# Kernel tuning notes

Measured on AMD Instinct MI355X. Metric: run time of the kernel, lower is better.

Reference implementation:

```python
import jax, jax.numpy as jnp
import numpy as np

B, H, C, Q = 32, 128, 2048, 256
NEG = -1e30


def setup_inputs() -> dict:
    key = jax.random.key(0)
    ks = jax.random.split(key, 8)
    context = jax.random.normal(ks[0], (B, H, C), dtype=jnp.float32)
    question = jax.random.normal(ks[1], (B, H, Q), dtype=jnp.float32)
    context_word_mask = jax.random.randint(ks[2], (B, C), 0, 2).astype(jnp.int32)
    question_word_mask = jax.random.randint(ks[3], (B, Q), 0, 2).astype(jnp.int32)
    # trilinear similarity params (QANet): S = c.w_c + q.w_q + (c*q).w_cq + bias
    scale = 1.0 / np.sqrt(H)
    w_c = jax.random.normal(ks[4], (H,), dtype=jnp.float32) * scale
    w_q = jax.random.normal(ks[5], (H,), dtype=jnp.float32) * scale
    w_cq = jax.random.normal(ks[6], (H,), dtype=jnp.float32) * scale
    bias = jnp.zeros((), dtype=jnp.float32)
    return {"context": context, "question": question,
            "context_word_mask": context_word_mask,
            "question_word_mask": question_word_mask,
            "w_c": w_c, "w_q": w_q, "w_cq": w_cq, "bias": bias}


def reference(context, question, context_word_mask, question_word_mask, w_c, w_q, w_cq, bias):
    # context: [B,H,C], question: [B,H,Q]
    # Trilinear similarity S[b,i,j] without materializing tiled [B,C,Q,H] tensors:
    part_c = jnp.einsum('bhi,h->bi', context, w_c)            # [B,C]
    part_q = jnp.einsum('bhj,h->bj', question, w_q)           # [B,Q]
    part_cq = jnp.einsum('bhi,bhj->bij', context * w_cq[None, :, None], question)  # [B,C,Q]
    S = part_cq + part_c[:, :, None] + part_q[:, None, :] + bias  # [B,C,Q]

    q_mask = question_word_mask[:, None, :].astype(bool)      # [B,1,Q]
    c_mask = context_word_mask[:, :, None].astype(bool)       # [B,C,1]
    S_row_norm = jax.nn.softmax(jnp.where(q_mask, S, NEG), axis=2)      # softmax over Q
    S_col_norm_T = jnp.swapaxes(jax.nn.softmax(jnp.where(c_mask, S, NEG), axis=1), 1, 2)  # [B,Q,C]

    context_t = jnp.swapaxes(context, 1, 2)    # [B,C,H]
    question_t = jnp.swapaxes(question, 1, 2)  # [B,Q,H]

    c2q = jnp.swapaxes(jnp.einsum('bij,bjh->bih', S_row_norm, question_t), 1, 2)  # [B,H,C]
    q2c = jnp.swapaxes(
        jnp.einsum('bik,bkh->bih', jnp.einsum('bij,bjk->bik', S_row_norm, S_col_norm_T), context_t),
        1, 2)  # [B,H,C]
    return (context, c2q, context * c2q, context * q2c)
```

## Files before the change

### kernel.cpp

```cpp
#include <hip/hip_runtime.h>
#include <hip/hip_bf16.h>
#include <math.h>


constexpr int kB = 32, kH = 128, kC = 2048, kQ = 256;
constexpr int kColChunks = 128;
constexpr float kNEG = -1e30f;

typedef short bf16x8 __attribute__((ext_vector_type(8)));
typedef float f32x4 __attribute__((ext_vector_type(4)));

static __device__ __forceinline__ unsigned short f2bf(float f) {
    __hip_bfloat16 h = __float2bfloat16(f);
    return __builtin_bit_cast(unsigned short, h);
}
static __device__ __forceinline__ float bf2f(unsigned short u) {
    unsigned int x = ((unsigned int)u) << 16;
    return __builtin_bit_cast(float, x);
}

__global__ __launch_bounds__(256) void k_prep_c(const float* __restrict__ ctx,
                                                const float* __restrict__ w_c,
                                                const float* __restrict__ w_cq,
                                                unsigned short* __restrict__ ctxW,
                                                float* __restrict__ part_c) {
    int i0 = blockIdx.x * 64, b = blockIdx.y;
    __shared__ unsigned short tile[64 * 136];
    __shared__ float pcp[4][64];
    int t = threadIdx.x;
    int il = t & 63, hg = t >> 6, hb = hg * 2;
    float accc = 0.f;
#pragma unroll
    for (int r = 0; r < 16; ++r) {
        int h = r * 8 + hb;
        float v0 = ctx[((size_t)b * kH + h) * kC + i0 + il];
        float v1 = ctx[((size_t)b * kH + h + 1) * kC + i0 + il];
        accc += v0 * w_c[h] + v1 * w_c[h + 1];
        unsigned int pk = (unsigned int)f2bf(v0 * w_cq[h]) |
                          ((unsigned int)f2bf(v1 * w_cq[h + 1]) << 16);
        *(unsigned int*)&tile[il * 136 + h] = pk;
    }
    pcp[hg][il] = accc;
    __syncthreads();
    if (t < 64) part_c[b * kC + i0 + t] = pcp[0][t] + pcp[1][t] + pcp[2][t] + pcp[3][t];
#pragma unroll
    for (int r = 0; r < 4; ++r) {
        int idx = r * 256 + t;
        int i = idx >> 4, hc = (idx & 15) * 8;
        *(bf16x8*)&ctxW[((size_t)b * kC + i0 + i) * kH + hc] =
            *(const bf16x8*)&tile[i * 136 + hc];
    }
}

__global__ __launch_bounds__(256) void k_prep_q(const float* __restrict__ q,
                                                const float* __restrict__ w_q,
                                                unsigned short* __restrict__ qT,
                                                unsigned short* __restrict__ qB,
                                                float* __restrict__ part_q) {
    int j0 = blockIdx.x * 64, b = blockIdx.y;
    __shared__ unsigned short tile[64 * 136];
    __shared__ float pcp[4][64];
    int t = threadIdx.x;
    int jl = t & 63, hg = t >> 6, hb = hg * 2;
    float accq = 0.f;
#pragma unroll
    for (int r = 0; r < 16; ++r) {
        int h = r * 8 + hb;
        float v0 = q[((size_t)b * kH + h) * kQ + j0 + jl];
        float v1 = q[((size_t)b * kH + h + 1) * kQ + j0 + jl];
        accq += v0 * w_q[h] + v1 * w_q[h + 1];
        qB[((size_t)b * kH + h) * kQ + j0 + jl]     = f2bf(v0);
        qB[((size_t)b * kH + h + 1) * kQ + j0 + jl] = f2bf(v1);
        unsigned int pk = (unsigned int)f2bf(v0) | ((unsigned int)f2bf(v1) << 16);
        *(unsigned int*)&tile[jl * 136 + h] = pk;
    }
    pcp[hg][jl] = accq;
    __syncthreads();
    if (t < 64) part_q[b * kQ + j0 + t] = pcp[0][t] + pcp[1][t] + pcp[2][t] + pcp[3][t];
#pragma unroll
    for (int r = 0; r < 4; ++r) {
        int idx = r * 256 + t;
        int j = idx >> 4, hc = (idx & 15) * 8;
        *(bf16x8*)&qT[((size_t)b * kQ + j0 + j) * kH + hc] =
            *(const bf16x8*)&tile[j * 136 + hc];
    }
}

__global__ __launch_bounds__(256) void k_Ssoft(const unsigned short* __restrict__ ctxW,
                                               const unsigned short* __restrict__ qT,
                                               const float* __restrict__ part_c,
                                               const float* __restrict__ part_q,
                                               const float* __restrict__ bias,
                                               const int* __restrict__ qmask,
                                               const int* __restrict__ cmask,
                                               unsigned short* __restrict__ RNb,
                                               float* __restrict__ rowscale,
                                               float* __restrict__ ps) {
    int i0 = blockIdx.x * 64, b = blockIdx.y;
    __shared__ unsigned short As[64 * 40];
    __shared__ unsigned short Bs[256 * 40];
    __shared__ float smpq[256];
    __shared__ int smqm[256];
    int t = threadIdx.x;
    int lane = t & 63, w = t >> 6;
    int lrow = lane & 15, q4 = lane >> 4, kgrp = q4 * 8;
    smpq[t] = part_q[b * kQ + t];
    smqm[t] = qmask[b * kQ + t];

    f32x4 acc[16];
#pragma unroll
    for (int nt = 0; nt < 16; ++nt) acc[nt] = (f32x4){0.f, 0.f, 0.f, 0.f};

    for (int kk = 0; kk < 4; ++kk) {
        int h0 = kk * 32;
        {
            int iA = t >> 2, hcA = (t & 3) * 8;
            *(bf16x8*)&As[iA * 40 + hcA] =
                *(const bf16x8*)&ctxW[((size_t)b * kC + i0 + iA) * kH + h0 + hcA];
        }
#pragma unroll
        for (int r2 = 0; r2 < 4; ++r2) {
            int idx = r2 * 256 + t;
            int jB = idx >> 2, hcB = (idx & 3) * 8;
            *(bf16x8*)&Bs[jB * 40 + hcB] =
                *(const bf16x8*)&qT[((size_t)b * kQ + jB) * kH + h0 + hcB];
        }
        __syncthreads();
        bf16x8 af = *(const bf16x8*)&As[(w * 16 + lrow) * 40 + kgrp];
#pragma unroll
        for (int nt = 0; nt < 16; ++nt) {
            bf16x8 bf = *(const bf16x8*)&Bs[(nt * 16 + lrow) * 40 + kgrp];
            acc[nt] = __builtin_amdgcn_mfma_f32_16x16x32_bf16(af, bf, acc[nt], 0, 0, 0);
        }
        __syncthreads();
    }

    float bs = bias[0];
    float pq[16];
    int qm[16];
#pragma unroll
    for (int nt = 0; nt < 16; ++nt) {
        int col = nt * 16 + lrow;
        pq[nt] = smpq[col];
        qm[nt] = smqm[col];
    }
    int rowbase = i0 + w * 16 + q4 * 4;
    float pc[4];
    int cmr[4];
#pragma unroll
    for (int r = 0; r < 4; ++r) {
        pc[r] = part_c[b * kC + rowbase + r] + bs;
        cmr[r] = cmask[b * kC + rowbase + r];
    }
#pragma unroll
    for (int nt = 0; nt < 16; ++nt)
#pragma unroll
        for (int r = 0; r < 4; ++r)
            acc[nt][r] += pc[r] + pq[nt];

    float cs[16];
#pragma unroll
    for (int nt = 0; nt < 16; ++nt) cs[nt] = 0.f;

#pragma unroll
    for (int r = 0; r < 4; ++r) {
        float rmax = kNEG;
#pragma unroll
        for (int nt = 0; nt < 16; ++nt)
            if (qm[nt]) rmax = fmaxf(rmax, acc[nt][r]);
        rmax = fmaxf(rmax, __shfl_xor(rmax, 1));
        rmax = fmaxf(rmax, __shfl_xor(rmax, 2));
        rmax = fmaxf(rmax, __shfl_xor(rmax, 4));
        rmax = fmaxf(rmax, __shfl_xor(rmax, 8));
        float e[16];
        float rsum = 0.f;
#pragma unroll
        for (int nt = 0; nt < 16; ++nt) {
            e[nt] = qm[nt] ? __expf(acc[nt][r] - rmax) : 0.f;
            rsum += e[nt];
        }
        rsum += __shfl_xor(rsum, 1);
        rsum += __shfl_xor(rsum, 2);
        rsum += __shfl_xor(rsum, 4);
        rsum += __shfl_xor(rsum, 8);
        float rinv = 1.f / rsum;
        float emax = __expf(rmax);
        unsigned short* dst = RNb + ((size_t)b * kC + rowbase + r) * kQ;
#pragma unroll
        for (int nt = 0; nt < 16; ++nt)
            dst[nt * 16 + lrow] = f2bf(e[nt] * rinv);
        if (lrow == 0)
            rowscale[b * kC + rowbase + r] = rsum * emax;
        if (cmr[r]) {
#pragma unroll
            for (int nt = 0; nt < 16; ++nt)
                cs[nt] += e[nt] * emax;
        }
    }
#pragma unroll
    for (int nt = 0; nt < 16; ++nt) {
        cs[nt] += __shfl_xor(cs[nt], 16);
        cs[nt] += __shfl_xor(cs[nt], 32);
    }
    int chunk = blockIdx.x * 4 + w;
#pragma unroll
    for (int k = 0; k < 4; ++k) {
        int nt = q4 * 4 + k;
        int col = nt * 16 + lrow;
        ps[((size_t)b * kColChunks + chunk) * kQ + col] = cs[nt];
    }
}

__global__ __launch_bounds__(256) void k_colZ(const float* __restrict__ ps,
                                              float* __restrict__ colinv) {
    int id = blockIdx.x * 256 + threadIdx.x;
    int b = id / kQ, j = id % kQ;
    float s = 0.f;
#pragma unroll 8
    for (int c = 0; c < kColChunks; ++c)
        s += ps[((size_t)b * kColChunks + c) * kQ + j];
    colinv[id] = s > 0.f ? 1.f / s : 0.f;
}

__global__ __launch_bounds__(256) void k_T2_mfma(const unsigned short* __restrict__ RNb,
                                                 const float* __restrict__ ctx,
                                                 const int* __restrict__ cmask,
                                                 const float* __restrict__ rowscale,
                                                 float* __restrict__ Tpart) {
    int chunk = blockIdx.x, jt = blockIdx.y, b = blockIdx.z;
    int j0 = jt * 128;
    __shared__ unsigned short Et[128 * 40];
    __shared__ unsigned short Bs[128 * 40];
    __shared__ int smc[256];
    int t = threadIdx.x;
    smc[t] = cmask[b * kC + chunk * 256 + t];
    int lane = t & 63, wave = t >> 6;
    int wm = wave >> 1, wn = wave & 1;
    int lrow = lane & 15, kgrp = (lane >> 4) * 8;
    int ip = t >> 4, js = t & 15;
    int hB = t >> 1, isegB = (t & 1) * 16;

    f32x4 acc[4][4];
#pragma unroll
    for (int mt = 0; mt < 4; ++mt)
#pragma unroll
        for (int nt = 0; nt < 4; ++nt)
            acc[mt][nt] = (f32x4){0.f, 0.f, 0.f, 0.f};
    __syncthreads();

    for (int kk = 0; kk < 8; ++kk) {
        int i0 = chunk * 256 + kk * 32;
        int li = kk * 32 + 2 * ip;
        float rs0 = smc[li]     ? rowscale[b * kC + chunk * 256 + li]     : 0.f;
        float rs1 = smc[li + 1] ? rowscale[b * kC + chunk * 256 + li + 1] : 0.f;
        const unsigned short* r0 = RNb + ((size_t)b * kC + i0 + 2 * ip) * kQ + j0;
#pragma unroll
        for (int m = 0; m < 8; ++m) {
            int j = js + 16 * m;
            float e0 = bf2f(r0[j]) * rs0;
            float e1 = bf2f(r0[kQ + j]) * rs1;
            unsigned int pk = (unsigned int)f2bf(e0) | ((unsigned int)f2bf(e1) << 16);
            *(unsigned int*)&Et[j * 40 + 2 * ip] = pk;
        }
        {
            const float* cb = ctx + ((size_t)b * kH + hB) * kC + i0 + isegB;
            float4 a0 = *(const float4*)cb;
            float4 a1 = *(const float4*)(cb + 4);
            float4 a2 = *(const float4*)(cb + 8);
            float4 a3 = *(const float4*)(cb + 12);
            float vv[16] = {a0.x, a0.y, a0.z, a0.w, a1.x, a1.y, a1.z, a1.w,
                            a2.x, a2.y, a2.z, a2.w, a3.x, a3.y, a3.z, a3.w};
            bf16x8 p0, p1;
#pragma unroll
            for (int e = 0; e < 8; ++e) {
                p0[e] = (short)f2bf(vv[e]);
                p1[e] = (short)f2bf(vv[8 + e]);
            }
            *(bf16x8*)&Bs[hB * 40 + isegB]     = p0;
            *(bf16x8*)&Bs[hB * 40 + isegB + 8] = p1;
        }
        __syncthreads();
        bf16x8 af[4], bfr[4];
#pragma unroll
        for (int mt = 0; mt < 4; ++mt)
            af[mt] = *(const bf16x8*)&Bs[(wm * 64 + mt * 16 + lrow) * 40 + kgrp];
#pragma unroll
        for (int nt = 0; nt < 4; ++nt)
            bfr[nt] = *(const bf16x8*)&Et[(wn * 64 + nt * 16 + lrow) * 40 + kgrp];
#pragma unroll
        for (int nt = 0; nt < 4; ++nt)
#pragma unroll
            for (int mt = 0; mt < 4; ++mt)
                acc[mt][nt] = __builtin_amdgcn_mfma_f32_16x16x32_bf16(af[mt], bfr[nt], acc[mt][nt], 0, 0, 0);
        __syncthreads();
    }

    const size_t M = (size_t)kB * kH * kQ;
#pragma unroll
    for (int mt = 0; mt < 4; ++mt)
#pragma unroll
        for (int r = 0; r < 4; ++r) {
            int h = wm * 64 + mt * 16 + (lane >> 4) * 4 + r;
            float* dst = Tpart + (size_t)chunk * M + ((size_t)b * kH + h) * kQ + j0 + wn * 64 + lrow;
#pragma unroll
            for (int nt = 0; nt < 4; ++nt)
                dst[nt * 16] = acc[mt][nt][r];
        }
}

__global__ __launch_bounds__(256) void k_Tred(const float* __restrict__ Tpart,
                                              const float* __restrict__ colinv,
                                              unsigned short* __restrict__ Tb) {
    size_t id = (size_t)blockIdx.x * 256 + threadIdx.x;
    const size_t M = (size_t)kB * kH * kQ;
    int j = (int)(id % kQ);
    int b = (int)(id / ((size_t)kH * kQ));
    float s = 0.f;
#pragma unroll
    for (int c = 0; c < 8; ++c) s += Tpart[c * M + id];
    Tb[id] = f2bf(s * colinv[b * kQ + j]);
}

__global__ __launch_bounds__(256) void k_out_mfma(const unsigned short* __restrict__ RNb,
                                                  const unsigned short* __restrict__ qB,
                                                  const unsigned short* __restrict__ Tb,
                                                  const float* __restrict__ ctx,
                                                  float* __restrict__ out) {
    int i0 = blockIdx.x * 64;
    int b  = blockIdx.y;
    __shared__ unsigned short As[64 * 40];
    __shared__ float stgC[64 * 68];
    __shared__ float stgT[64 * 68];
    int t = threadIdx.x;
    int rA = t >> 2, cA = (t & 3) * 8;
    int lane = t & 63, wave = t >> 6;
    int hw = wave * 32;
    int kgrp = (lane >> 4) * 8;
    int lrow = lane & 15, q4 = lane >> 4;

    f32x4 accC[4][2];
    f32x4 accT[4][2];
#pragma unroll
    for (int mt = 0; mt < 4; ++mt)
#pragma unroll
        for (int nt = 0; nt < 2; ++nt) {
            accC[mt][nt] = (f32x4){0.f, 0.f, 0.f, 0.f};
            accT[mt][nt] = (f32x4){0.f, 0.f, 0.f, 0.f};
        }

    for (int kk = 0; kk < 8; ++kk) {
        int j0 = kk * 32;
        *(bf16x8*)&As[rA * 40 + cA] =
            *(const bf16x8*)&RNb[((size_t)b * kC + i0 + rA) * kQ + j0 + cA];
        __syncthreads();
        bf16x8 af[4];
#pragma unroll
        for (int mt = 0; mt < 4; ++mt)
            af[mt] = *(const bf16x8*)&As[(mt * 16 + lrow) * 40 + kgrp];
#pragma unroll
        for (int nt = 0; nt < 2; ++nt) {
            int h = hw + nt * 16 + lrow;
            bf16x8 bq = *(const bf16x8*)&qB[((size_t)b * kH + h) * kQ + j0 + kgrp];
            bf16x8 bt = *(const bf16x8*)&Tb[((size_t)b * kH + h) * kQ + j0 + kgrp];
#pragma unroll
            for (int mt = 0; mt < 4; ++mt) {
                accC[mt][nt] = __builtin_amdgcn_mfma_f32_16x16x32_bf16(af[mt], bq, accC[mt][nt], 0, 0, 0);
                accT[mt][nt] = __builtin_amdgcn_mfma_f32_16x16x32_bf16(af[mt], bt, accT[mt][nt], 0, 0, 0);
            }
        }
        __syncthreads();
    }

    const size_t N = (size_t)kB * kH * kC;
    int ii = t & 63, hb = t >> 6;
#pragma unroll
    for (int g = 0; g < 2; ++g) {
        if ((wave >> 1) == g) {
            int hloc = (wave & 1) * 32;
#pragma unroll
            for (int mt = 0; mt < 4; ++mt)
#pragma unroll
                for (int nt = 0; nt < 2; ++nt)
#pragma unroll
                    for (int r = 0; r < 4; ++r) {
                        int rowh = hloc + nt * 16 + lrow;
                        int coli = mt * 16 + q4 * 4 + r;
                        stgC[rowh * 68 + coli] = accC[mt][nt][r];
                        stgT[rowh * 68 + coli] = accT[mt][nt][r];
                    }
        }
        __syncthreads();
#pragma unroll 4
        for (int p = 0; p < 16; ++p) {
            int hl = hb + p * 4;
            int h = g * 64 + hl;
            float vc = stgC[hl * 68 + ii];
            float vt = stgT[hl * 68 + ii];
            size_t base = ((size_t)b * kH + h) * kC + i0 + ii;
            float c = ctx[base];
            out[base]         = c;
            out[N + base]     = vc;
            out[2 * N + base] = c * vc;
            out[3 * N + base] = c * vt;
        }
        __syncthreads();
    }
}

extern "C" void kernel_launch(void* const* d_in, const int* in_sizes, int n_in,
                              void* d_out, int out_size, void* d_ws, size_t ws_size,
                              hipStream_t stream) {
    const float* ctx   = (const float*)d_in[0];
    const float* q     = (const float*)d_in[1];
    const int*   cmask = (const int*)d_in[2];
    const int*   qmask = (const int*)d_in[3];
    const float* w_c   = (const float*)d_in[4];
    const float* w_q   = (const float*)d_in[5];
    const float* w_cq  = (const float*)d_in[6];
    const float* bias  = (const float*)d_in[7];
    float* out = (float*)d_out;

    unsigned short* RNb = (unsigned short*)d_ws;
    unsigned short* qB  = RNb + (size_t)kB * kC * kQ;
    unsigned short* Tb  = qB + (size_t)kB * kH * kQ;
    float* part_c   = (float*)(Tb + (size_t)kB * kH * kQ);
    float* part_q   = part_c + kB * kC;
    float* rowscale = part_q + kB * kQ;
    float* colinv   = rowscale + kB * kC;
    float* ps       = colinv + kB * kQ;
    size_t need = (size_t)((char*)(ps + (size_t)kB * kColChunks * kQ) - (char*)d_ws);
    if (ws_size < need) return;

    const size_t N = (size_t)kB * kH * kC;
    float* Tpart = out;
    unsigned short* ctxW = (unsigned short*)(out + 2 * N);
    unsigned short* qT   = ctxW + (size_t)kB * kC * kH;

    k_prep_c<<<dim3(kC / 64, kB), 256, 0, stream>>>(ctx, w_c, w_cq, ctxW, part_c);
    k_prep_q<<<dim3(kQ / 64, kB), 256, 0, stream>>>(q, w_q, qT, qB, part_q);
    k_Ssoft<<<dim3(kC / 64, kB), 256, 0, stream>>>(ctxW, qT, part_c, part_q, bias,
                                                   qmask, cmask, RNb, rowscale, ps);
    k_colZ<<<kB * kQ / 256, 256, 0, stream>>>(ps, colinv);
    k_T2_mfma<<<dim3(8, 2, kB), 256, 0, stream>>>(RNb, ctx, cmask, rowscale, Tpart);
    k_Tred<<<kB * kH * kQ / 256, 256, 0, stream>>>(Tpart, colinv, Tb);
    k_out_mfma<<<dim3(kC / 64, kB), 256, 0, stream>>>(RNb, qB, Tb, ctx, out);
}
```

Baseline: 119.3 us.

## Store unnormalized exp scores and bf16 context; apply row normalization at output

```diff
diff --git a/kernel.cpp b/kernel.cpp
--- a/kernel.cpp
+++ b/kernel.cpp
@@ -13,16 +13,13 @@
 static __device__ __forceinline__ unsigned short f2bf(float f) {
     __hip_bfloat16 h = __float2bfloat16(f);
     return __builtin_bit_cast(unsigned short, h);
-}
-static __device__ __forceinline__ float bf2f(unsigned short u) {
-    unsigned int x = ((unsigned int)u) << 16;
-    return __builtin_bit_cast(float, x);
 }
 
 __global__ __launch_bounds__(256) void k_prep_c(const float* __restrict__ ctx,
                                                 const float* __restrict__ w_c,
                                                 const float* __restrict__ w_cq,
                                                 unsigned short* __restrict__ ctxW,
+                                                unsigned short* __restrict__ ctxB,
                                                 float* __restrict__ part_c) {
     int i0 = blockIdx.x * 64, b = blockIdx.y;
     __shared__ unsigned short tile[64 * 136];
@@ -36,6 +33,8 @@
         float v0 = ctx[((size_t)b * kH + h) * kC + i0 + il];
         float v1 = ctx[((size_t)b * kH + h + 1) * kC + i0 + il];
         accc += v0 * w_c[h] + v1 * w_c[h + 1];
+        ctxB[((size_t)b * kH + h) * kC + i0 + il]     = f2bf(v0);
+        ctxB[((size_t)b * kH + h + 1) * kC + i0 + il] = f2bf(v1);
         unsigned int pk = (unsigned int)f2bf(v0 * w_cq[h]) |
                           ((unsigned int)f2bf(v1 * w_cq[h + 1]) << 16);
         *(unsigned int*)&tile[il * 136 + h] = pk;
@@ -93,8 +92,8 @@
                                                const float* __restrict__ bias,
                                                const int* __restrict__ qmask,
                                                const int* __restrict__ cmask,
-                                               unsigned short* __restrict__ RNb,
-                                               float* __restrict__ rowscale,
+                                               unsigned short* __restrict__ Eb,
+                                               float* __restrict__ rowinv,
                                                float* __restrict__ ps) {
     int i0 = blockIdx.x * 64, b = blockIdx.y;
     __shared__ unsigned short As[64 * 40];
@@ -183,14 +182,14 @@
         rsum += __shfl_xor(rsum, 2);
         rsum += __shfl_xor(rsum, 4);
         rsum += __shfl_xor(rsum, 8);
-        float rinv = 1.f / rsum;
         float emax = __expf(rmax);
-        unsigned short* dst = RNb + ((size_t)b * kC + rowbase + r) * kQ;
+        float Z = rsum * emax;
+        unsigned short* dst = Eb + ((size_t)b * kC + rowbase + r) * kQ;
 #pragma unroll
         for (int nt = 0; nt < 16; ++nt)
-            dst[nt * 16 + lrow] = f2bf(e[nt] * rinv);
+            dst[nt * 16 + lrow] = f2bf(e[nt] * emax);
         if (lrow == 0)
-            rowscale[b * kC + rowbase + r] = rsum * emax;
+            rowinv[b * kC + rowbase + r] = Z > 0.f ? 1.f / Z : 0.f;
         if (cmr[r]) {
 #pragma unroll
             for (int nt = 0; nt < 16; ++nt)
@@ -222,10 +221,9 @@
     colinv[id] = s > 0.f ? 1.f / s : 0.f;
 }
 
-__global__ __launch_bounds__(256) void k_T2_mfma(const unsigned short* __restrict__ RNb,
-                                                 const float* __restrict__ ctx,
+__global__ __launch_bounds__(256) void k_T2_mfma(const unsigned short* __restrict__ Eb,
+                                                 const unsigned short* __restrict__ ctxB,
                                                  const int* __restrict__ cmask,
-                                                 const float* __restrict__ rowscale,
                                                  float* __restrict__ Tpart) {
     int chunk = blockIdx.x, jt = blockIdx.y, b = blockIdx.z;
     int j0 = jt * 128;
@@ -251,33 +249,20 @@
     for (int kk = 0; kk < 8; ++kk) {
         int i0 = chunk * 256 + kk * 32;
         int li = kk * 32 + 2 * ip;
-        float rs0 = smc[li]     ? rowscale[b * kC + chunk * 256 + li]     : 0.f;
-        float rs1 = smc[li + 1] ? rowscale[b * kC + chunk * 256 + li + 1] : 0.f;
-        const unsigned short* r0 = RNb + ((size_t)b * kC + i0 + 2 * ip) * kQ + j0;
+        unsigned int m0 = smc[li]     ? 0xFFFFu : 0u;
+        unsigned int m1 = smc[li + 1] ? 0xFFFFu : 0u;
+        const unsigned short* r0 = Eb + ((size_t)b * kC + i0 + 2 * ip) * kQ + j0;
 #pragma unroll
         for (int m = 0; m < 8; ++m) {
             int j = js + 16 * m;
-            float e0 = bf2f(r0[j]) * rs0;
-            float e1 = bf2f(r0[kQ + j]) * rs1;
-            unsigned int pk = (unsigned int)f2bf(e0) | ((unsigned int)f2bf(e1) << 16);
-            *(unsigned int*)&Et[j * 40 + 2 * ip] = pk;
+            unsigned int e0 = (unsigned int)r0[j] & m0;
+            unsigned int e1 = (unsigned int)r0[kQ + j] & m1;
+            *(unsigned int*)&Et[j * 40 + 2 * ip] = e0 | (e1 << 16);
         }
         {
-            const float* cb = ctx + ((size_t)b * kH + hB) * kC + i0 + isegB;
-            float4 a0 = *(const float4*)cb;
-            float4 a1 = *(const float4*)(cb + 4);
-            float4 a2 = *(const float4*)(cb + 8);
-            float4 a3 = *(const float4*)(cb + 12);
-            float vv[16] = {a0.x, a0.y, a0.z, a0.w, a1.x, a1.y, a1.z, a1.w,
-                            a2.x, a2.y, a2.z, a2.w, a3.x, a3.y, a3.z, a3.w};
-            bf16x8 p0, p1;
-#pragma unroll
-            for (int e = 0; e < 8; ++e) {
-                p0[e] = (short)f2bf(vv[e]);
-                p1[e] = (short)f2bf(vv[8 + e]);
-            }
-            *(bf16x8*)&Bs[hB * 40 + isegB]     = p0;
-            *(bf16x8*)&Bs[hB * 40 + isegB + 8] = p1;
+            const unsigned short* cb = ctxB + ((size_t)b * kH + hB) * kC + i0 + isegB;
+            *(bf16x8*)&Bs[hB * 40 + isegB]     = *(const bf16x8*)cb;
+            *(bf16x8*)&Bs[hB * 40 + isegB + 8] = *(const bf16x8*)(cb + 8);
         }
         __syncthreads();
         bf16x8 af[4], bfr[4];
@@ -321,10 +306,11 @@
     Tb[id] = f2bf(s * colinv[b * kQ + j]);
 }
 
-__global__ __launch_bounds__(256) void k_out_mfma(const unsigned short* __restrict__ RNb,
+__global__ __launch_bounds__(256) void k_out_mfma(const unsigned short* __restrict__ Eb,
                                                   const unsigned short* __restrict__ qB,
                                                   const unsigned short* __restrict__ Tb,
                                                   const float* __restrict__ ctx,
+                                                  const float* __restrict__ rowinv,
                                                   float* __restrict__ out) {
     int i0 = blockIdx.x * 64;
     int b  = blockIdx.y;
@@ -351,7 +337,7 @@
     for (int kk = 0; kk < 8; ++kk) {
         int j0 = kk * 32;
         *(bf16x8*)&As[rA * 40 + cA] =
-            *(const bf16x8*)&RNb[((size_t)b * kC + i0 + rA) * kQ + j0 + cA];
+            *(const bf16x8*)&Eb[((size_t)b * kC + i0 + rA) * kQ + j0 + cA];
         __syncthreads();
         bf16x8 af[4];
 #pragma unroll
@@ -373,6 +359,7 @@
 
     const size_t N = (size_t)kB * kH * kC;
     int ii = t & 63, hb = t >> 6;
+    float riv = rowinv[b * kC + i0 + ii];
 #pragma unroll
     for (int g = 0; g < 2; ++g) {
         if ((wave >> 1) == g) {
@@ -394,8 +381,8 @@
         for (int p = 0; p < 16; ++p) {
             int hl = hb + p * 4;
             int h = g * 64 + hl;
-            float vc = stgC[hl * 68 + ii];
-            float vt = stgT[hl * 68 + ii];
+            float vc = stgC[hl * 68 + ii] * riv;
+            float vt = stgT[hl * 68 + ii] * riv;
             size_t base = ((size_t)b * kH + h) * kC + i0 + ii;
             float c = ctx[base];
             out[base]         = c;
@@ -420,14 +407,15 @@
     const float* bias  = (const float*)d_in[7];
     float* out = (float*)d_out;
 
-    unsigned short* RNb = (unsigned short*)d_ws;
-    unsigned short* qB  = RNb + (size_t)kB * kC * kQ;
-    unsigned short* Tb  = qB + (size_t)kB * kH * kQ;
-    float* part_c   = (float*)(Tb + (size_t)kB * kH * kQ);
-    float* part_q   = part_c + kB * kC;
-    float* rowscale = part_q + kB * kQ;
-    float* colinv   = rowscale + kB * kC;
-    float* ps       = colinv + kB * kQ;
+    unsigned short* Eb   = (unsigned short*)d_ws;
+    unsigned short* ctxB = Eb + (size_t)kB * kC * kQ;
+    unsigned short* qB   = ctxB + (size_t)kB * kH * kC;
+    unsigned short* Tb   = qB + (size_t)kB * kH * kQ;
+    float* part_c = (float*)(Tb + (size_t)kB * kH * kQ);
+    float* part_q = part_c + kB * kC;
+    float* rowinv = part_q + kB * kQ;
+    float* colinv = rowinv + kB * kC;
+    float* ps     = colinv + kB * kQ;
     size_t need = (size_t)((char*)(ps + (size_t)kB * kColChunks * kQ) - (char*)d_ws);
     if (ws_size < need) return;
 
@@ -436,12 +424,12 @@
     unsigned short* ctxW = (unsigned short*)(out + 2 * N);
     unsigned short* qT   = ctxW + (size_t)kB * kC * kH;
 
-    k_prep_c<<<dim3(kC / 64, kB), 256, 0, stream>>>(ctx, w_c, w_cq, ctxW, part_c);
+    k_prep_c<<<dim3(kC / 64, kB), 256, 0, stream>>>(ctx, w_c, w_cq, ctxW, ctxB, part_c);
     k_prep_q<<<dim3(kQ / 64, kB), 256, 0, stream>>>(q, w_q, qT, qB, part_q);
     k_Ssoft<<<dim3(kC / 64, kB), 256, 0, stream>>>(ctxW, qT, part_c, part_q, bias,
-                                                   qmask, cmask, RNb, rowscale, ps);
+                                                   qmask, cmask, Eb, rowinv, ps);
     k_colZ<<<kB * kQ / 256, 256, 0, stream>>>(ps, colinv);
-    k_T2_mfma<<<dim3(8, 2, kB), 256, 0, stream>>>(RNb, ctx, cmask, rowscale, Tpart);
+    k_T2_mfma<<<dim3(8, 2, kB), 256, 0, stream>>>(Eb, ctxB, cmask, Tpart);
     k_Tred<<<kB * kH * kQ / 256, 256, 0, stream>>>(Tpart, colinv, Tb);
-    k_out_mfma<<<dim3(kC / 64, kB), 256, 0, stream>>>(RNb, qB, Tb, ctx, out);
-}
+    k_out_mfma<<<dim3(kC / 64, kB), 256, 0, stream>>>(Eb, qB, Tb, ctx, rowinv, out);
+}
```

Result: slower. 129.4 us (+8.5%).
